# Kernel tuning notes

Measured on AMD Instinct MI355X. Metric: run time of the kernel, lower is better.

## Reference

```python
import jax, jax.numpy as jnp
import numpy as np

I = 512
D = 256
C = 10          # num_clusters
E = 8           # cluster_emb_dim
NCLS = 2
NEG = -1e9

def _xavier(key, shape):
    fan_in, fan_out = shape[0], shape[1]
    std = np.sqrt(2.0 / (fan_in + fan_out))
    return jax.random.normal(key, shape, dtype=jnp.float32) * std

def setup_inputs() -> dict:
    key = jax.random.key(0)
    ks = jax.random.split(key, 16)
    B, N = 8, 8192
    h = jax.random.normal(ks[0], (B, N, I), dtype=jnp.float32)
    cluster_ids = jax.random.randint(ks[1], (B, N), 0, C)
    return {
        "h": h,
        "cluster_ids": cluster_ids,
        "emb_table": jax.random.normal(ks[2], (C, E), dtype=jnp.float32) * 0.02,
        "Wf": _xavier(ks[3], (I + E, I)), "bf": jnp.zeros((I,), jnp.float32),
        # intra gated attention
        "Wa": _xavier(ks[4], (I, D)), "ba": jnp.zeros((D,), jnp.float32),
        "Wb": _xavier(ks[5], (I, D)), "bb": jnp.zeros((D,), jnp.float32),
        "Wc": _xavier(ks[6], (D, 1)), "bc": jnp.zeros((1,), jnp.float32),
        "Wfc": _xavier(ks[7], (I, 512)), "bfc": jnp.zeros((512,), jnp.float32),
        # inter gated attention
        "Wa2": _xavier(ks[8], (512, D)), "ba2": jnp.zeros((D,), jnp.float32),
        "Wb2": _xavier(ks[9], (512, D)), "bb2": jnp.zeros((D,), jnp.float32),
        "Wc2": _xavier(ks[10], (D, 1)), "bc2": jnp.zeros((1,), jnp.float32),
        "Wfc2": _xavier(ks[11], (512, 256)), "bfc2": jnp.zeros((256,), jnp.float32),
        "Wcls": _xavier(ks[12], (256, NCLS)), "bcls": jnp.zeros((NCLS,), jnp.float32),
    }

def reference(h, cluster_ids, emb_table, Wf, bf, Wa, ba, Wb, bb, Wc, bc,
              Wfc, bfc, Wa2, ba2, Wb2, bb2, Wc2, bc2, Wfc2, bfc2, Wcls, bcls):
    # 1) fuse cluster embedding: concat + Linear + ReLU  -> [B,N,I]
    emb = emb_table[cluster_ids]                              # [B,N,E]
    x = jnp.concatenate([h, emb], axis=-1)                    # [B,N,I+E]
    x = jax.nn.relu(jnp.einsum('bnf,fi->bni', x, Wf) + bf)    # [B,N,I]

    # 2) intra-cluster gated attention scores (shared MLP over all patches)
    a = jnp.tanh(jnp.einsum('bni,id->bnd', x, Wa) + ba)
    g = jax.nn.sigmoid(jnp.einsum('bni,id->bnd', x, Wb) + bb)
    s = (jnp.einsum('bnd,do->bno', a * g, Wc) + bc)[..., 0]   # [B,N]

    # segmented softmax per (batch, cluster): mask then softmax over N
    m = cluster_ids[:, :, None] == jnp.arange(C)[None, None, :]  # [B,N,C] bool
    sm = jnp.where(m, s[:, :, None], NEG)
    A = jax.nn.softmax(sm, axis=1)                             # [B,N,C]

    # weighted sum per cluster -> [B,C,I], then intra_fc -> [B,C,512]
    cfeat = jnp.einsum('bnc,bni->bci', A, x)
    cfeat = jax.nn.relu(jnp.einsum('bci,io->bco', cfeat, Wfc) + bfc)

    # 3) inter-cluster gated attention over C clusters
    a2 = jnp.tanh(jnp.einsum('bcf,fd->bcd', cfeat, Wa2) + ba2)
    g2 = jax.nn.sigmoid(jnp.einsum('bcf,fd->bcd', cfeat, Wb2) + bb2)
    s2 = (jnp.einsum('bcd,do->bco', a2 * g2, Wc2) + bc2)[..., 0]  # [B,C]
    A2 = jax.nn.softmax(s2, axis=1)                               # [B,C]
    slide = jnp.einsum('bc,bcf->bf', A2, cfeat)                   # [B,512]
    slide = jax.nn.relu(slide @ Wfc2 + bfc2)                      # [B,256]

    # 4) classifier
    logits = slide @ Wcls + bcls                                  # [B,n_classes]
    return logits
```

## Files before the change

kernel.cpp:

```cpp
#include <hip/hip_runtime.h>
#include <math.h>

#define B_    8
#define N_    8192
#define M_    65536
#define I_    512
#define E_    8
#define D_    256
#define C_    10
#define NCLS_ 2

typedef unsigned short ushort_t;
typedef ushort_t ushortx8 __attribute__((ext_vector_type(8)));
typedef __bf16   bf16x8  __attribute__((ext_vector_type(8)));
typedef float    f32x4   __attribute__((ext_vector_type(4)));

static const size_t XB_OFF   = 0;
static const size_t PS_OFF   = 67108864;
static const size_t S_OFF    = PS_OFF + 2097152;
static const size_t PST_OFF  = S_OFF + 262144;
static const size_t CP_OFF   = PST_OFF + 5120;
static const size_t CF2_OFF  = CP_OFF + 10485760;
static const size_t S2_OFF   = CF2_OFF + 163840;
static const size_t WFT_OFF  = S2_OFF + 512;
static const size_t BAG_OFF  = WFT_OFF + 524288;
static const size_t EMBW_OFF = BAG_OFF + 524288;

__device__ __forceinline__ float sigf(float v) { return 1.0f / (1.0f + __expf(-v)); }

__device__ __forceinline__ ushort_t f2bf(float f) {
    union { float f; unsigned u; } v; v.f = f;
    unsigned r = v.u + 0x7FFF + ((v.u >> 16) & 1);
    return (ushort_t)(r >> 16);
}
__device__ __forceinline__ float bf2f(ushort_t u) {
    union { unsigned u; float f; } v; v.u = ((unsigned)u) << 16; return v.f;
}

__device__ __forceinline__ void gl_lds16(const void* g, void* l) {
    __builtin_amdgcn_global_load_lds(
        (const __attribute__((address_space(1))) void*)g,
        (__attribute__((address_space(3))) void*)l, 16, 0, 0);
}

#define VMWAIT5 asm volatile("s_waitcnt vmcnt(5)" ::: "memory")
#define VMWAIT3 asm volatile("s_waitcnt vmcnt(3)" ::: "memory")
#define VMWAIT0 asm volatile("s_waitcnt vmcnt(0)" ::: "memory")
#define CFENCE  asm volatile("" ::: "memory")

__global__ __launch_bounds__(256) void prep_kernel(
    const float* __restrict__ Wf, const float* __restrict__ Wa,
    const float* __restrict__ Wb, const float* __restrict__ emb,
    const float* __restrict__ bfv,
    ushort_t* __restrict__ wft, ushort_t* __restrict__ bag,
    float* __restrict__ embW)
{
    const int bid = blockIdx.x;
    const int t = threadIdx.x;
    if (bid < 1024) {
        int idx = bid * 256 + t;
        int k = idx >> 9, n = idx & 511;
        wft[(size_t)n * 512 + k] = f2bf(Wf[(size_t)k * 512 + n]);
    } else if (bid < 1536) {
        int idx = (bid - 1024) * 256 + t;
        int k = idx >> 8, d = idx & 255;
        float a = Wa[(size_t)k * 256 + d];
        float g = Wb[(size_t)k * 256 + d];
        int blk = d >> 5, w = d & 31;
        bag[(size_t)(blk * 64 + w) * 512 + k]      = f2bf(a);
        bag[(size_t)(blk * 64 + 32 + w) * 512 + k] = f2bf(g);
    } else {
        int idx = (bid - 1536) * 256 + t;
        int c = idx >> 9, n = idx & 511;
        float s = bfv[n];
#pragma unroll
        for (int e = 0; e < 8; ++e) s += emb[c * 8 + e] * Wf[(size_t)(512 + e) * 512 + n];
        embW[(size_t)c * 512 + n] = s;
    }
}

__global__ __launch_bounds__(512) void gemm_x_mfma(
    const float* __restrict__ hf, const int* __restrict__ cid,
    const ushort_t* __restrict__ wft, const float* __restrict__ embW,
    ushort_t* __restrict__ xb)
{
    __shared__ float    Asf[3][256 * 32];
    __shared__ ushort_t Bs[3][128 * 32];

    const int t = threadIdx.x;
    const int lin = blockIdx.y * 4 + blockIdx.x;
    const int swz = (lin & 7) * 128 + (lin >> 3);
    const int n0 = (swz & 3) * 128;
    const int m0 = (swz >> 2) * 256;

    const int wid = t >> 6;
    const int wr = wid >> 1, wc = wid & 1;
    const int l = t & 63, lr = l & 15, lg = l >> 4;

    const int srow = l >> 2;
    const int gchB = ((l & 3) ^ ((l >> 3) & 3)) * 8;
    const size_t gB0 = (size_t)(n0 + wid * 16 + srow) * 512 + gchB;

    const int ArowL = wid * 32 + (l >> 3);
    const int gchA  = ((l & 7) ^ ((l >> 3) & 7)) * 4;
    const size_t gAf = (size_t)(m0 + ArowL) * 512 + gchA;

    f32x4 acc[4][4] = {};

#define STAGE_X(buf, kt) do { \
    size_t ko = (size_t)(kt) * 32; \
    char* aB = (char*)&Asf[buf][0] + wid * 4096; \
    gl_lds16(hf + gAf + ko,            aB); \
    gl_lds16(hf + gAf + ko +  8 * 512, aB + 1024); \
    gl_lds16(hf + gAf + ko + 16 * 512, aB + 2048); \
    gl_lds16(hf + gAf + ko + 24 * 512, aB + 3072); \
    gl_lds16(wft + gB0 + ko, &Bs[buf][wid * 512]); \
} while (0)

    STAGE_X(0, 0);
    STAGE_X(1, 1);
    for (int kt = 0; kt < 16; ++kt) {
        if (kt < 15) { VMWAIT5; } else { VMWAIT0; }
        __builtin_amdgcn_s_barrier();
        CFENCE;
        if (kt + 2 < 16) STAGE_X((kt + 2) % 3, kt + 2);
        const float* Aw = &Asf[kt % 3][0];
        const char*  Bb = (const char*)&Bs[kt % 3][0];
        bf16x8 af[4], bg[4];
#pragma unroll
        for (int mi = 0; mi < 4; ++mi) {
            int R = wr * 64 + mi * 16 + lr;
            const float* Arow = Aw + R * 32;
            int s7 = R & 7;
            f32x4 lo = *(const f32x4*)(Arow + (((2 * lg)     ^ s7) << 2));
            f32x4 hi = *(const f32x4*)(Arow + (((2 * lg + 1) ^ s7) << 2));
            bf16x8 a;
            a[0] = (__bf16)lo[0]; a[1] = (__bf16)lo[1];
            a[2] = (__bf16)lo[2]; a[3] = (__bf16)lo[3];
            a[4] = (__bf16)hi[0]; a[5] = (__bf16)hi[1];
            a[6] = (__bf16)hi[2]; a[7] = (__bf16)hi[3];
            af[mi] = a;
        }
#pragma unroll
        for (int ni = 0; ni < 4; ++ni) {
            int Cc = wc * 64 + ni * 16 + lr;
            bg[ni] = *(const bf16x8*)(Bb + Cc * 64 + ((lg ^ ((Cc >> 1) & 3)) << 4));
        }
#pragma unroll
        for (int mi = 0; mi < 4; ++mi)
#pragma unroll
            for (int ni = 0; ni < 4; ++ni)
                acc[mi][ni] = __builtin_amdgcn_mfma_f32_16x16x32_bf16(af[mi], bg[ni], acc[mi][ni], 0, 0, 0);
    }
    __syncthreads();

    ushort_t* sc = (ushort_t*)&Asf[0][0];
#pragma unroll
    for (int mi = 0; mi < 4; ++mi) {
#pragma unroll
        for (int r = 0; r < 4; ++r) {
            int row = wr * 64 + mi * 16 + lg * 4 + r;
            const float* ew = embW + (size_t)cid[m0 + row] * 512;
#pragma unroll
            for (int ni = 0; ni < 4; ++ni) {
                int col = wc * 64 + ni * 16 + lr;
                float v = acc[mi][ni][r] + ew[n0 + col];
                sc[row * 128 + col] = f2bf(fmaxf(v, 0.0f));
            }
        }
    }
    __syncthreads();
    {
        const int cch = t & 15;
        const int r0  = t >> 4;
#pragma unroll
        for (int j = 0; j < 8; ++j) {
            int row = r0 + j * 32;
            *(ushortx8*)(xb + (size_t)(m0 + row) * 512 + n0 + cch * 8) =
                *(const ushortx8*)(sc + row * 128 + cch * 8);
        }
    }
}

__global__ __launch_bounds__(512) void gemm_ag_mfma(
    const ushort_t* __restrict__ xb, const ushort_t* __restrict__ bag,
    const float* __restrict__ bav, const float* __restrict__ bbv,
    const float* __restrict__ Wc, float* __restrict__ ps)
{
    __shared__ ushort_t As[3][256 * 32];
    __shared__ ushort_t Bs[3][128 * 32];

    const int t = threadIdx.x;
    const int lin = blockIdx.y * 4 + blockIdx.x;
    const int swz = (lin & 7) * 128 + (lin >> 3);
    const int bxn = swz & 3;
    const int n0 = bxn * 128;
    const int m0 = (swz >> 2) * 256;

    const int wid = t >> 6;
    const int wr = wid >> 1, wc = wid & 1;
    const int l = t & 63, lr = l & 15, lg = l >> 4;

    const int srow = l >> 2;
    const int gch  = ((l & 3) ^ ((l >> 3) & 3)) * 8;

    const size_t gA0 = (size_t)(m0 + wid * 32 + srow) * 512 + gch;
    const size_t gA1 = gA0 + 16 * 512;
    const size_t gB0 = (size_t)(n0 + wid * 16 + srow) * 512 + gch;

    f32x4 acc[4][4] = {};

#define STAGE_AG(buf, kt) do { \
    size_t ko = (size_t)(kt) * 32; \
    gl_lds16(xb + gA0 + ko,  &As[buf][wid * 1024]); \
    gl_lds16(xb + gA1 + ko,  &As[buf][wid * 1024 + 512]); \
    gl_lds16(bag + gB0 + ko, &Bs[buf][wid * 512]); \
} while (0)

    STAGE_AG(0, 0);
    STAGE_AG(1, 1);
    for (int kt = 0; kt < 16; ++kt) {
        if (kt < 15) { VMWAIT3; } else { VMWAIT0; }
        __builtin_amdgcn_s_barrier();
        CFENCE;
        if (kt + 2 < 16) STAGE_AG((kt + 2) % 3, kt + 2);
        const char* Ab = (const char*)&As[kt % 3][0];
        const char* Bb = (const char*)&Bs[kt % 3][0];
        bf16x8 af[4], bg[4];
#pragma unroll
        for (int mi = 0; mi < 4; ++mi) {
            int R = wr * 64 + mi * 16 + lr;
            af[mi] = *(const bf16x8*)(Ab + R * 64 + ((lg ^ ((R >> 1) & 3)) << 4));
        }
#pragma unroll
        for (int ni = 0; ni < 4; ++ni) {
            int Cc = wc * 64 + ni * 16 + lr;
            bg[ni] = *(const bf16x8*)(Bb + Cc * 64 + ((lg ^ ((Cc >> 1) & 3)) << 4));
        }
#pragma unroll
        for (int mi = 0; mi < 4; ++mi)
#pragma unroll
            for (int ni = 0; ni < 4; ++ni)
                acc[mi][ni] = __builtin_amdgcn_mfma_f32_16x16x32_bf16(af[mi], bg[ni], acc[mi][ni], 0, 0, 0);
    }

    const int blk = bxn * 2 + wc;
    const int d0 = blk * 32 + lr, d1 = d0 + 16;
    const float ba0 = bav[d0], ba1 = bav[d1];
    const float bb0 = bbv[d0], bb1 = bbv[d1];
    const float w0 = Wc[d0],  w1 = Wc[d1];

#pragma unroll
    for (int mi = 0; mi < 4; ++mi) {
#pragma unroll
        for (int r = 0; r < 4; ++r) {
            float p = tanhf(acc[mi][0][r] + ba0) * sigf(acc[mi][2][r] + bb0) * w0
                    + tanhf(acc[mi][1][r] + ba1) * sigf(acc[mi][3][r] + bb1) * w1;
            p += __shfl_xor(p, 1); p += __shfl_xor(p, 2);
            p += __shfl_xor(p, 4); p += __shfl_xor(p, 8);
            if (lr == 0)
                ps[(size_t)blk * M_ + m0 + wr * 64 + mi * 16 + lg * 4 + r] = p;
        }
    }
}

__global__ __launch_bounds__(256) void sstats_kernel(
    const float* __restrict__ ps, const float* __restrict__ bc,
    const int* __restrict__ cid, float* __restrict__ S,
    float* __restrict__ pst)
{
    __shared__ float redm[4][C_];
    __shared__ float smx[C_];
    __shared__ float reds[4][C_];

    const int b  = blockIdx.x >> 3;
    const int sl = blockIdx.x & 7;
    const int bs = blockIdx.x;
    const int t  = threadIdx.x;
    const int l  = t & 63, wv = t >> 6;
    const int base = b * N_ + sl * 1024;

    float sv[4]; int cv[4];
#pragma unroll
    for (int i = 0; i < 4; ++i) {
        int m = base + i * 256 + t;
        float v = bc[0];
#pragma unroll
        for (int k = 0; k < 8; ++k) v += ps[(size_t)k * M_ + m];
        S[m] = v; sv[i] = v; cv[i] = cid[m];
    }

    float mx[C_];
#pragma unroll
    for (int c = 0; c < C_; ++c) mx[c] = -3.0e38f;
#pragma unroll
    for (int i = 0; i < 4; ++i)
#pragma unroll
        for (int c = 0; c < C_; ++c)
            mx[c] = fmaxf(mx[c], (cv[i] == c) ? sv[i] : -3.0e38f);
#pragma unroll
    for (int c = 0; c < C_; ++c) {
        float v = mx[c];
        v = fmaxf(v, __shfl_xor(v, 32)); v = fmaxf(v, __shfl_xor(v, 16));
        v = fmaxf(v, __shfl_xor(v, 8));  v = fmaxf(v, __shfl_xor(v, 4));
        v = fmaxf(v, __shfl_xor(v, 2));  v = fmaxf(v, __shfl_xor(v, 1));
        if (l == 0) redm[wv][c] = v;
    }
    __syncthreads();
    if (t < C_)
        smx[t] = fmaxf(fmaxf(redm[0][t], redm[1][t]), fmaxf(redm[2][t], redm[3][t]));
    __syncthreads();

    float sm[C_];
#pragma unroll
    for (int c = 0; c < C_; ++c) sm[c] = 0.f;
#pragma unroll
    for (int i = 0; i < 4; ++i) {
        float e = expf(sv[i] - smx[cv[i]]);
#pragma unroll
        for (int c = 0; c < C_; ++c) sm[c] += (cv[i] == c) ? e : 0.f;
    }
#pragma unroll
    for (int c = 0; c < C_; ++c) {
        float v = sm[c];
        v += __shfl_xor(v, 32); v += __shfl_xor(v, 16); v += __shfl_xor(v, 8);
        v += __shfl_xor(v, 4);  v += __shfl_xor(v, 2);  v += __shfl_xor(v, 1);
        if (l == 0) reds[wv][c] = v;
    }
    __syncthreads();
    if (t < C_) {
        pst[bs * C_ + t]       = smx[t];
        pst[640 + bs * C_ + t] = reds[0][t] + reds[1][t] + reds[2][t] + reds[3][t];
    }
}

__global__ __launch_bounds__(256) void cpart_kernel(
    const ushort_t* __restrict__ xb, const int* __restrict__ cid,
    const float* __restrict__ s, const float* __restrict__ pst,
    float* __restrict__ cpart)
{
    __shared__ float smax[C_], sinv[C_];
    __shared__ float wrow[128];
    __shared__ int   crow[128];
    const int b     = blockIdx.x >> 6;
    const int chunk = blockIdx.x & 63;
    const int t     = threadIdx.x;
    const int base  = b * N_ + chunk * 128;

    if (t < C_) {
        float mxv = -3.0e38f;
#pragma unroll
        for (int sl = 0; sl < 8; ++sl)
            mxv = fmaxf(mxv, pst[(b * 8 + sl) * C_ + t]);
        float sum = 0.f;
#pragma unroll
        for (int sl = 0; sl < 8; ++sl)
            sum += pst[640 + (b * 8 + sl) * C_ + t] * expf(pst[(b * 8 + sl) * C_ + t] - mxv);
        smax[t] = mxv;
        sinv[t] = 1.0f / sum;
    }
    __syncthreads();
    if (t < 128) {
        int m = base + t;
        int c = cid[m];
        crow[t] = c;
        wrow[t] = expf(s[m] - smax[c]) * sinv[c];
    }
    __syncthreads();

    float2 acc[C_];
#pragma unroll
    for (int c = 0; c < C_; ++c) { acc[c].x = 0.f; acc[c].y = 0.f; }

    for (int r = 0; r < 128; ++r) {
        int c = crow[r];
        float wv = wrow[r];
        unsigned xv = *(const unsigned*)(xb + (size_t)(base + r) * 512 + t * 2);
        float x0 = bf2f((ushort_t)(xv & 0xffff));
        float x1 = bf2f((ushort_t)(xv >> 16));
#pragma unroll
        for (int cc = 0; cc < C_; ++cc) {
            float w = (cc == c) ? wv : 0.0f;
            acc[cc].x += w * x0;
            acc[cc].y += w * x1;
        }
    }
#pragma unroll
    for (int cc = 0; cc < C_; ++cc)
        *(float2*)(&cpart[(((size_t)blockIdx.x) * C_ + cc) * 512 + t * 2]) = acc[cc];
}

__global__ __launch_bounds__(256) void intra_inter_kernel(
    const float* __restrict__ cpart, const float* __restrict__ Wfc,
    const float* __restrict__ bfc,
    const float* __restrict__ Wa2, const float* __restrict__ ba2,
    const float* __restrict__ Wb2, const float* __restrict__ bb2,
    const float* __restrict__ Wc2, const float* __restrict__ bc2,
    float* __restrict__ cfeat2, float* __restrict__ s2)
{
    __shared__ float row[512];
    __shared__ float row2[512];
    __shared__ float red[256];
    const int bc = blockIdx.x;
    const int b = bc / C_, c = bc % C_;
    const int t  = threadIdx.x;

    float r0 = 0.f, r1 = 0.f;
    for (int ch = 0; ch < 64; ++ch) {
        size_t o = (((size_t)(b * 64 + ch)) * C_ + c) * 512;
        r0 += cpart[o + t];
        r1 += cpart[o + 256 + t];
    }
    row[t] = r0; row[t + 256] = r1;
    __syncthreads();

    float a0 = 0.f, a1 = 0.f;
    for (int i = 0; i < 512; ++i) {
        float rv = row[i];
        a0 += rv * Wfc[(size_t)i * 512 + t];
        a1 += rv * Wfc[(size_t)i * 512 + 256 + t];
    }
    a0 = fmaxf(a0 + bfc[t], 0.f);
    a1 = fmaxf(a1 + bfc[256 + t], 0.f);
    cfeat2[bc * 512 + t]       = a0;
    cfeat2[bc * 512 + 256 + t] = a1;
    row2[t] = a0; row2[t + 256] = a1;
    __syncthreads();

    float pa = 0.f, pg = 0.f;
    for (int f = 0; f < 512; ++f) {
        float rv = row2[f];
        pa += rv * Wa2[(size_t)f * 256 + t];
        pg += rv * Wb2[(size_t)f * 256 + t];
    }
    float v = tanhf(pa + ba2[t]) * sigf(pg + bb2[t]) * Wc2[t];
    red[t] = v; __syncthreads();
    for (int off = 128; off > 0; off >>= 1) {
        if (t < off) red[t] += red[t + off];
        __syncthreads();
    }
    if (t == 0) s2[bc] = red[0] + bc2[0];
}

__global__ __launch_bounds__(256) void final_kernel(
    const float* __restrict__ cfeat2, const float* __restrict__ s2,
    const float* __restrict__ Wfc2, const float* __restrict__ bfc2,
    const float* __restrict__ Wcls, const float* __restrict__ bcls,
    float* __restrict__ out)
{
    __shared__ float A2[C_];
    __shared__ float slide[512];
    __shared__ float slide2[256];
    const int b = blockIdx.x;
    const int t = threadIdx.x;

    if (t < C_) A2[t] = s2[b * C_ + t];
    __syncthreads();
    float mx = -3.0e38f;
    for (int c = 0; c < C_; ++c) mx = fmaxf(mx, A2[c]);
    float sum = 0.f;
    for (int c = 0; c < C_; ++c) sum += expf(A2[c] - mx);
    __syncthreads();
    if (t < C_) A2[t] = expf(A2[t] - mx) / sum;
    __syncthreads();

    float s0 = 0.f, s1 = 0.f;
    for (int c = 0; c < C_; ++c) {
        float a = A2[c];
        s0 += a * cfeat2[(b * C_ + c) * 512 + t];
        s1 += a * cfeat2[(b * C_ + c) * 512 + 256 + t];
    }
    slide[t] = s0; slide[t + 256] = s1;
    __syncthreads();

    float acc = 0.f;
    for (int f = 0; f < 512; ++f) acc += slide[f] * Wfc2[(size_t)f * 256 + t];
    slide2[t] = fmaxf(acc + bfc2[t], 0.f);
    __syncthreads();

    if (t < NCLS_) {
        float lg = bcls[t];
        for (int o = 0; o < 256; ++o) lg += slide2[o] * Wcls[o * 2 + t];
        out[b * 2 + t] = lg;
    }
}

extern "C" void kernel_launch(void* const* d_in, const int* in_sizes, int n_in,
                              void* d_out, int out_size, void* d_ws, size_t ws_size,
                              hipStream_t stream)
{
    (void)in_sizes; (void)n_in; (void)out_size; (void)ws_size;
    const float* h    = (const float*)d_in[0];
    const int*   cid  = (const int*)  d_in[1];
    const float* emb  = (const float*)d_in[2];
    const float* Wf   = (const float*)d_in[3];
    const float* bf   = (const float*)d_in[4];
    const float* Wa   = (const float*)d_in[5];
    const float* ba   = (const float*)d_in[6];
    const float* Wb   = (const float*)d_in[7];
    const float* bb   = (const float*)d_in[8];
    const float* Wc   = (const float*)d_in[9];
    const float* bc   = (const float*)d_in[10];
    const float* Wfc  = (const float*)d_in[11];
    const float* bfc  = (const float*)d_in[12];
    const float* Wa2  = (const float*)d_in[13];
    const float* ba2  = (const float*)d_in[14];
    const float* Wb2  = (const float*)d_in[15];
    const float* bb2  = (const float*)d_in[16];
    const float* Wc2  = (const float*)d_in[17];
    const float* bc2  = (const float*)d_in[18];
    const float* Wfc2 = (const float*)d_in[19];
    const float* bfc2 = (const float*)d_in[20];
    const float* Wcls = (const float*)d_in[21];
    const float* bcls = (const float*)d_in[22];

    char* ws = (char*)d_ws;
    ushort_t* XB   = (ushort_t*)(ws + XB_OFF);
    float* PS      = (float*)(ws + PS_OFF);
    float* S       = (float*)(ws + S_OFF);
    float* PST     = (float*)(ws + PST_OFF);
    float* CPART   = (float*)(ws + CP_OFF);
    float* CFEAT2  = (float*)(ws + CF2_OFF);
    float* S2      = (float*)(ws + S2_OFF);
    ushort_t* WFT  = (ushort_t*)(ws + WFT_OFF);
    ushort_t* BAG  = (ushort_t*)(ws + BAG_OFF);
    float* EMBW    = (float*)(ws + EMBW_OFF);
    float* out     = (float*)d_out;

    prep_kernel<<<1556, 256, 0, stream>>>(Wf, Wa, Wb, emb, bf, WFT, BAG, EMBW);

    gemm_x_mfma<<<dim3(4, 256), 512, 0, stream>>>(h, cid, WFT, EMBW, XB);
    gemm_ag_mfma<<<dim3(4, 256), 512, 0, stream>>>(XB, BAG, ba, bb, Wc, PS);

    sstats_kernel<<<64, 256, 0, stream>>>(PS, bc, cid, S, PST);
    cpart_kernel<<<512, 256, 0, stream>>>(XB, cid, S, PST, CPART);
    intra_inter_kernel<<<B_ * C_, 256, 0, stream>>>(CPART, Wfc, bfc,
                                                    Wa2, ba2, Wb2, bb2, Wc2, bc2,
                                                    CFEAT2, S2);
    final_kernel<<<B_, 256, 0, stream>>>(CFEAT2, S2, Wfc2, bfc2, Wcls, bcls, out);
}
```

Measured before the change: 251.4 us.

## Use double-buffered LDS pipeline in x GEMM and tile the Wf transpose

The main x-projection GEMM drops from a three-stage asynchronous LDS pipeline with explicit vmcnt waits to a two-stage double buffer synchronised by __syncthreads each k-step. This cuts LDS per block from about 120KB to 80KB, so two 512-thread blocks may fit per CU. The cost is that loads for the next tile overlap less with compute. Separately, the prep kernel's Wf transpose now goes through a padded 64x64 shared-memory tile, so both the read and the bf16 write are coalesced and the prep launch needs fewer blocks.

After: 223.1 us. 11.3% less time.

```diff
diff --git a/kernel.cpp b/kernel.cpp
--- a/kernel.cpp
+++ b/kernel.cpp
@@ -43,7 +43,6 @@
         (__attribute__((address_space(3))) void*)l, 16, 0, 0);
 }
 
-#define VMWAIT5 asm volatile("s_waitcnt vmcnt(5)" ::: "memory")
 #define VMWAIT3 asm volatile("s_waitcnt vmcnt(3)" ::: "memory")
 #define VMWAIT0 asm volatile("s_waitcnt vmcnt(0)" ::: "memory")
 #define CFENCE  asm volatile("" ::: "memory")
@@ -55,14 +54,26 @@
     ushort_t* __restrict__ wft, ushort_t* __restrict__ bag,
     float* __restrict__ embW)
 {
+    __shared__ float tile[64][65];
     const int bid = blockIdx.x;
     const int t = threadIdx.x;
-    if (bid < 1024) {
-        int idx = bid * 256 + t;
-        int k = idx >> 9, n = idx & 511;
-        wft[(size_t)n * 512 + k] = f2bf(Wf[(size_t)k * 512 + n]);
-    } else if (bid < 1536) {
-        int idx = (bid - 1024) * 256 + t;
+    if (bid < 64) {
+        const int ti = bid >> 3, tj = bid & 7;
+#pragma unroll
+        for (int i = 0; i < 16; ++i) {
+            int kl = i * 4 + (t >> 6);
+            int nl = t & 63;
+            tile[nl][kl] = Wf[(size_t)(ti * 64 + kl) * 512 + tj * 64 + nl];
+        }
+        __syncthreads();
+#pragma unroll
+        for (int i = 0; i < 16; ++i) {
+            int nl = i * 4 + (t >> 6);
+            int kl = t & 63;
+            wft[(size_t)(tj * 64 + nl) * 512 + ti * 64 + kl] = f2bf(tile[nl][kl]);
+        }
+    } else if (bid < 576) {
+        int idx = (bid - 64) * 256 + t;
         int k = idx >> 8, d = idx & 255;
         float a = Wa[(size_t)k * 256 + d];
         float g = Wb[(size_t)k * 256 + d];
@@ -70,7 +81,7 @@
         bag[(size_t)(blk * 64 + w) * 512 + k]      = f2bf(a);
         bag[(size_t)(blk * 64 + 32 + w) * 512 + k] = f2bf(g);
     } else {
-        int idx = (bid - 1536) * 256 + t;
+        int idx = (bid - 576) * 256 + t;
         int c = idx >> 9, n = idx & 511;
         float s = bfv[n];
 #pragma unroll
@@ -84,8 +95,8 @@
     const ushort_t* __restrict__ wft, const float* __restrict__ embW,
     ushort_t* __restrict__ xb)
 {
-    __shared__ float    Asf[3][256 * 32];
-    __shared__ ushort_t Bs[3][128 * 32];
+    __shared__ float    Asf[2][256 * 32];
+    __shared__ ushort_t Bs[2][128 * 32];
 
     const int t = threadIdx.x;
     const int lin = blockIdx.y * 4 + blockIdx.x;
@@ -100,6 +111,7 @@
     const int srow = l >> 2;
     const int gchB = ((l & 3) ^ ((l >> 3) & 3)) * 8;
     const size_t gB0 = (size_t)(n0 + wid * 16 + srow) * 512 + gchB;
+    ushort_t* lB = &Bs[0][wid * 512];
 
     const int ArowL = wid * 32 + (l >> 3);
     const int gchA  = ((l & 7) ^ ((l >> 3) & 7)) * 4;
@@ -114,18 +126,16 @@
     gl_lds16(hf + gAf + ko +  8 * 512, aB + 1024); \
     gl_lds16(hf + gAf + ko + 16 * 512, aB + 2048); \
     gl_lds16(hf + gAf + ko + 24 * 512, aB + 3072); \
-    gl_lds16(wft + gB0 + ko, &Bs[buf][wid * 512]); \
+    gl_lds16(wft + gB0 + ko, lB + (buf) * 4096); \
 } while (0)
 
     STAGE_X(0, 0);
-    STAGE_X(1, 1);
+    __syncthreads();
+    int cur = 0;
     for (int kt = 0; kt < 16; ++kt) {
-        if (kt < 15) { VMWAIT5; } else { VMWAIT0; }
-        __builtin_amdgcn_s_barrier();
-        CFENCE;
-        if (kt + 2 < 16) STAGE_X((kt + 2) % 3, kt + 2);
-        const float* Aw = &Asf[kt % 3][0];
-        const char*  Bb = (const char*)&Bs[kt % 3][0];
+        if (kt < 15) STAGE_X(cur ^ 1, kt + 1);
+        const float* Aw = &Asf[cur][0];
+        const char*  Bb = (const char*)&Bs[cur][0];
         bf16x8 af[4], bg[4];
 #pragma unroll
         for (int mi = 0; mi < 4; ++mi) {
@@ -151,8 +161,9 @@
 #pragma unroll
             for (int ni = 0; ni < 4; ++ni)
                 acc[mi][ni] = __builtin_amdgcn_mfma_f32_16x16x32_bf16(af[mi], bg[ni], acc[mi][ni], 0, 0, 0);
-    }
-    __syncthreads();
+        __syncthreads();
+        cur ^= 1;
+    }
 
     ushort_t* sc = (ushort_t*)&Asf[0][0];
 #pragma unroll
@@ -527,7 +538,7 @@
     float* EMBW    = (float*)(ws + EMBW_OFF);
     float* out     = (float*)d_out;
 
-    prep_kernel<<<1556, 256, 0, stream>>>(Wf, Wa, Wb, emb, bf, WFT, BAG, EMBW);
+    prep_kernel<<<596, 256, 0, stream>>>(Wf, Wa, Wb, emb, bf, WFT, BAG, EMBW);
 
     gemm_x_mfma<<<dim3(4, 256), 512, 0, stream>>>(h, cid, WFT, EMBW, XB);
     gemm_ag_mfma<<<dim3(4, 256), 512, 0, stream>>>(XB, BAG, ba, bb, Wc, PS);
```
